# Performance work log

Hardware: AMD Instinct MI355X
Metric: run time of the kernel (lower is better)

## Reference

```python
import jax, jax.numpy as jnp
import numpy as np

N_NODES = 50000
N_EDGES = 800000
N_FEAT = 128
HIDDEN = 256
BN_EPS = 1e-5


def setup_inputs() -> dict:
    key = jax.random.key(0)
    ks = jax.random.split(key, 8)
    x = jax.random.normal(ks[0], (N_NODES, N_FEAT), dtype=jnp.float32)
    edge_index = jax.random.randint(ks[1], (2, N_EDGES), 0, N_NODES, dtype=jnp.int64)
    # Xavier-uniform linear weights (as in weights_init), zero biases
    def xavier(k, fan_in, fan_out):
        lim = float(np.sqrt(6.0 / (fan_in + fan_out)))
        return jax.random.uniform(k, (fan_in, fan_out), jnp.float32, -lim, lim)
    return {
        "x": x,
        "edge_index": edge_index,
        "W1": xavier(ks[2], N_FEAT, HIDDEN),
        "b1": jnp.zeros((HIDDEN,), jnp.float32),
        "g1": jnp.ones((HIDDEN,), jnp.float32),
        "be1": jnp.zeros((HIDDEN,), jnp.float32),
        "W2": xavier(ks[3], HIDDEN, HIDDEN),
        "b2": jnp.zeros((HIDDEN,), jnp.float32),
        "g2": jnp.ones((HIDDEN,), jnp.float32),
        "be2": jnp.zeros((HIDDEN,), jnp.float32),
        "Wfc": xavier(ks[4], HIDDEN, HIDDEN),
        "bfc": jnp.zeros((HIDDEN,), jnp.float32),
    }


def gcn_conv(x, src, dst, deg_inv_sqrt, W, b):
    """PyG GCNConv: out_i = sum_{j->i} d_i^-1/2 d_j^-1/2 (x_j W) + b,
    with self-loops already appended to (src, dst)."""
    h = x @ W                                        # [N, out]
    norm = deg_inv_sqrt[src] * deg_inv_sqrt[dst]     # [E+N]
    msgs = h[src] * norm[:, None]                    # gather + scale
    out = jax.ops.segment_sum(msgs, dst, num_segments=x.shape[0])
    return out + b


def batch_norm(x, gamma, beta):
    # training-mode BatchNorm1d: batch stats over nodes, biased variance
    mean = jnp.mean(x, axis=0)
    var = jnp.mean(jnp.square(x - mean), axis=0)
    return (x - mean) * jax.lax.rsqrt(var + BN_EPS) * gamma + beta


def reference(x, edge_index, W1, b1, g1, be1, W2, b2, g2, be2, Wfc, bfc):
    n = x.shape[0]
    loop = jnp.arange(n, dtype=edge_index.dtype)
    src = jnp.concatenate([edge_index[0], loop])
    dst = jnp.concatenate([edge_index[1], loop])
    deg = jax.ops.segment_sum(jnp.ones_like(src, dtype=x.dtype), dst, num_segments=n)
    deg_inv_sqrt = jnp.where(deg > 0, jax.lax.rsqrt(jnp.maximum(deg, 1.0)), 0.0)

    h = gcn_conv(x, src, dst, deg_inv_sqrt, W1, b1)
    h = batch_norm(h, g1, be1)
    # dropout is identity in deterministic (eval) reference
    h = gcn_conv(h, src, dst, deg_inv_sqrt, W2, b2)
    h = batch_norm(h, g2, be2)
    return h @ Wfc + bfc
```

## Files before the change

### kernel.cpp

```cpp
#include <hip/hip_runtime.h>
#include <hip/hip_bf16.h>

#define NFEAT 128
#define HID 256
#define BN_EPS 1e-5f
#define NBIN 64

typedef __attribute__((ext_vector_type(8))) __bf16 bf16x8;
typedef __attribute__((ext_vector_type(4))) float f32x4;

static __device__ __forceinline__ float bflo(unsigned u) {
    union { unsigned x; float f; } c; c.x = u << 16; return c.f;
}
static __device__ __forceinline__ float bfhi(unsigned u) {
    union { unsigned x; float f; } c; c.x = u & 0xffff0000u; return c.f;
}

__global__ void k_count(const int* __restrict__ ei, int E, int* __restrict__ cnt,
                        int* __restrict__ rank) {
    int e = blockIdx.x * blockDim.x + threadIdx.x;
    if (e < E) rank[e] = atomicAdd(&cnt[ei[E + e]], 1);
}

__global__ void k_scan1(const int* __restrict__ cnt, int n, int* __restrict__ partial,
                        int* __restrict__ blk_total) {
    __shared__ int sh[256];
    int i = blockIdx.x * 256 + threadIdx.x;
    int v = (i < n) ? cnt[i] : 0;
    sh[threadIdx.x] = v;
    __syncthreads();
    for (int off = 1; off < 256; off <<= 1) {
        int x = (threadIdx.x >= off) ? sh[threadIdx.x - off] : 0;
        __syncthreads();
        sh[threadIdx.x] += x;
        __syncthreads();
    }
    if (i < n) partial[i] = sh[threadIdx.x] - v;
    if (threadIdx.x == 255) blk_total[blockIdx.x] = sh[255];
}

__global__ void k_finalize(const int* __restrict__ partial, const int* __restrict__ blk_total,
                           const int* __restrict__ cnt, int n, int nblk,
                           int* __restrict__ row_start, float* __restrict__ dinv) {
    __shared__ int sw[4];
    const int t = threadIdx.x;
    const int b = blockIdx.x;
    int v = (t < b && t < nblk) ? blk_total[t] : 0;
#pragma unroll
    for (int m = 1; m < 64; m <<= 1) v += __shfl_xor(v, m);
    if ((t & 63) == 0) sw[t >> 6] = v;
    __syncthreads();
    int pref = sw[0] + sw[1] + sw[2] + sw[3];
    int i = b * 256 + t;
    if (i < n) {
        row_start[i] = partial[i] + pref;
        dinv[i] = rsqrtf((float)(cnt[i] + 1));
    }
}

__global__ void k_fill(const int* __restrict__ ei, const int* __restrict__ rank,
                       const int* __restrict__ row_start, int E, int* __restrict__ col) {
    int e = blockIdx.x * blockDim.x + threadIdx.x;
    if (e < E) {
        int d = ei[E + e];
        col[row_start[d] + rank[e]] = ei[e];
    }
}

__global__ void k_prep(const float* __restrict__ x, const float* __restrict__ dinv,
                       __hip_bfloat16* __restrict__ xs, const float* __restrict__ W1,
                       __hip_bfloat16* __restrict__ Wt1, int castBlocks, int n4) {
    int bid = blockIdx.x;
    int t = threadIdx.x;
    if (bid < castBlocks) {
        int i = bid * 256 + t;
        if (i < n4) {
            float d = dinv[i >> 5];
            float4 v = *(const float4*)(x + (size_t)i * 4);
            __hip_bfloat16* o = xs + (size_t)i * 4;
            o[0] = __float2bfloat16(v.x * d);
            o[1] = __float2bfloat16(v.y * d);
            o[2] = __float2bfloat16(v.z * d);
            o[3] = __float2bfloat16(v.w * d);
        }
    } else {
        int idx = (bid - castBlocks) * 256 + t;
        int n = idx & 255;
        int k = idx >> 8;
        Wt1[n * 128 + k] = __float2bfloat16(W1[k * 256 + n]);
    }
}

__global__ __launch_bounds__(256) void k_bnfoldW(const float* __restrict__ gs,
                                                 const float* __restrict__ g,
                                                 const float* __restrict__ be,
                                                 const float* __restrict__ b, float invN,
                                                 const float* __restrict__ W1,
                                                 const float* __restrict__ W2,
                                                 __hip_bfloat16* __restrict__ WfT,
                                                 float* __restrict__ uvec) {
    __shared__ float shs[256], shb[256];
    const int c = threadIdx.x;
    float s = 0.f, q = 0.f;
    for (int r = 0; r < NBIN; r++) {
        s += gs[r * 512 + c];
        q += gs[r * 512 + 256 + c];
    }
    float mean = s * invN;
    float var = q * invN - mean * mean;
    float scl = rsqrtf(var + BN_EPS) * g[c];
    shs[c] = scl;
    shb[c] = (b[c] - mean) * scl + be[c];
    __syncthreads();
    if (blockIdx.x < 128) {
        int k = blockIdx.x;
        float acc = 0.f;
        for (int m = 0; m < 256; m++) acc += W1[k * 256 + m] * shs[m] * W2[m * 256 + c];
        WfT[(size_t)c * 128 + k] = __float2bfloat16(acc);
    } else {
        float acc = 0.f;
        for (int m = 0; m < 256; m++) acc += W2[m * 256 + c] * shb[m];
        uvec[c] = acc;
    }
}

__global__ __launch_bounds__(256) void k_fold2(const float* __restrict__ gs,
                                               const float* __restrict__ g,
                                               const float* __restrict__ be, float invN,
                                               const float* __restrict__ Wfc,
                                               const float* __restrict__ bfc,
                                               __hip_bfloat16* __restrict__ Wtf,
                                               float* __restrict__ bias2) {
    __shared__ float shs[256], sho[256];
    const int c = threadIdx.x;
    float s = 0.f, q = 0.f;
    for (int r = 0; r < NBIN; r++) {
        s += gs[r * 512 + c];
        q += gs[r * 512 + 256 + c];
    }
    float mean = s * invN;
    float var = q * invN - mean * mean;
    float scl = rsqrtf(var + BN_EPS) * g[c];
    shs[c] = scl;
    sho[c] = (0.f - mean) * scl + be[c];
    __syncthreads();
    if (blockIdx.x < 256) {
        int k = blockIdx.x;
        Wtf[(size_t)c * 256 + k] = __float2bfloat16(Wfc[k * 256 + c] * shs[k]);
    } else {
        float acc = bfc[c];
        for (int m = 0; m < 256; m++) acc += sho[m] * Wfc[m * 256 + c];
        bias2[c] = acc;
    }
}

template <bool SCALE>
__global__ __launch_bounds__(256) void k_spmm(const __hip_bfloat16* __restrict__ Hs,
                                              const int* __restrict__ rs,
                                              const int* __restrict__ rc,
                                              const int* __restrict__ col,
                                              const float* __restrict__ dinv,
                                              __hip_bfloat16* __restrict__ out,
                                              float* __restrict__ rv, int N) {
    const int wid = blockIdx.x * 4 + (threadIdx.x >> 6);
    if (wid >= N) return;
    const int lane = threadIdx.x & 63;
    const int ch = lane * 2;
    const int s = rs[wid];
    const int deg = rc[wid];
    const float di = dinv[wid];

    unsigned u0 = *(const unsigned*)(Hs + (size_t)wid * 128 + ch);
    float a0, a1, dsum = 0.f;
    if constexpr (SCALE) { a0 = di * bflo(u0); a1 = di * bfhi(u0); }
    else { a0 = bflo(u0); a1 = bfhi(u0); }

    int e = 0;
    for (; e + 8 <= deg; e += 8) {
        int idx[8];
#pragma unroll
        for (int j = 0; j < 8; j++) idx[j] = col[s + e + j];
        float dj[8];
#pragma unroll
        for (int j = 0; j < 8; j++) dj[j] = dinv[idx[j]];
        unsigned u[8];
#pragma unroll
        for (int j = 0; j < 8; j++) u[j] = *(const unsigned*)(Hs + (size_t)idx[j] * 128 + ch);
#pragma unroll
        for (int j = 0; j < 8; j++) {
            if constexpr (SCALE) { a0 += dj[j] * bflo(u[j]); a1 += dj[j] * bfhi(u[j]); }
            else { a0 += bflo(u[j]); a1 += bfhi(u[j]); dsum += dj[j]; }
        }
    }
    for (; e < deg; e++) {
        int i0 = col[s + e];
        float d0 = dinv[i0];
        unsigned uu = *(const unsigned*)(Hs + (size_t)i0 * 128 + ch);
        if constexpr (SCALE) { a0 += d0 * bflo(uu); a1 += d0 * bfhi(uu); }
        else { a0 += bflo(uu); a1 += bfhi(uu); dsum += d0; }
    }
    union { unsigned w; unsigned short us[2]; } o;
    __hip_bfloat16 b0 = __float2bfloat16(di * a0); o.us[0] = *(unsigned short*)&b0;
    __hip_bfloat16 b1 = __float2bfloat16(di * a1); o.us[1] = *(unsigned short*)&b1;
    *(unsigned*)(out + (size_t)wid * 128 + ch) = o.w;
    if (!SCALE && rv && lane == 0) rv[wid] = di * (di + dsum);
}

template <int K, bool STATS>
__global__ __launch_bounds__(256, 4) void k_gemm2(const __hip_bfloat16* __restrict__ A,
                                                  const __hip_bfloat16* __restrict__ Bt,
                                                  const float* __restrict__ bias,
                                                  __hip_bfloat16* __restrict__ outb,
                                                  float* __restrict__ outf,
                                                  float* __restrict__ gs,
                                                  const float* __restrict__ rvec,
                                                  const float* __restrict__ uvec, int M) {
    constexpr int NC = K / 64;
    constexpr int LDR = 72;
    __shared__ __align__(16) unsigned short Bs[2 * 128 * LDR];
    float* sred = (float*)Bs;
    float* qred = sred + 512;

    const int t = threadIdx.x;
    const int wv = t >> 6;
    const int lane = t & 63;
    const int mlane = lane & 15;
    const int quad = lane >> 4;
    const int m0 = blockIdx.x * 128;
    const int n0 = blockIdx.y * 128;
    const int arow0 = m0 + wv * 32 + mlane;

    auto stage = [&](int c, int buf) {
#pragma unroll
        for (int i = 0; i < 4; i++) {
            int idx = t + i * 256;
            int row = idx >> 3;
            int c4 = idx & 7;
            uint4 v = *(const uint4*)(Bt + (size_t)(n0 + row) * K + c * 64 + c4 * 8);
            *(uint4*)(Bs + buf * (128 * LDR) + row * LDR + c4 * 8) = v;
        }
    };
    auto loadA = [&](int c, bf16x8 (&dst)[2][2]) {
#pragma unroll
        for (int mt = 0; mt < 2; mt++)
#pragma unroll
            for (int ks = 0; ks < 2; ks++)
                dst[mt][ks] = *(const bf16x8*)(A + (size_t)(arow0 + mt * 16) * K + c * 64 +
                                               ks * 32 + quad * 8);
    };

    f32x4 acc[2][8];
#pragma unroll
    for (int mt = 0; mt < 2; mt++)
#pragma unroll
        for (int i = 0; i < 8; i++) acc[mt][i] = (f32x4){0.f, 0.f, 0.f, 0.f};

    bf16x8 aP[2][2], aQ[2][2];
    loadA(0, aP);
    stage(0, 0);

    auto mmachunk = [&](int c, bf16x8 (&ac)[2][2]) {
        const unsigned short* base = Bs + (c & 1) * (128 * LDR);
#pragma unroll
        for (int nt = 0; nt < 8; nt++) {
            const unsigned short* bp = base + (nt * 16 + mlane) * LDR + quad * 8;
#pragma unroll
            for (int ks = 0; ks < 2; ks++) {
                bf16x8 b = *(const bf16x8*)(bp + ks * 32);
                acc[0][nt] = __builtin_amdgcn_mfma_f32_16x16x32_bf16(ac[0][ks], b, acc[0][nt], 0, 0, 0);
                acc[1][nt] = __builtin_amdgcn_mfma_f32_16x16x32_bf16(ac[1][ks], b, acc[1][nt], 0, 0, 0);
            }
        }
    };

#pragma unroll
    for (int c = 0; c < NC; c++) {
        __syncthreads();
        if (c + 1 < NC) {
            stage(c + 1, (c + 1) & 1);
            if ((c & 1) == 0) loadA(c + 1, aQ); else loadA(c + 1, aP);
        }
        if ((c & 1) == 0) mmachunk(c, aP); else mmachunk(c, aQ);
    }

    float rv[2][4] = {{0.f, 0.f, 0.f, 0.f}, {0.f, 0.f, 0.f, 0.f}};
    if (rvec) {
#pragma unroll
        for (int mt = 0; mt < 2; mt++)
#pragma unroll
            for (int r = 0; r < 4; r++) {
                int row = m0 + wv * 32 + mt * 16 + quad * 4 + r;
                if (row < M) rv[mt][r] = rvec[row];
            }
    }
    float sp[8], qp[8];
#pragma unroll
    for (int nt = 0; nt < 8; nt++) {
        int colx = n0 + nt * 16 + mlane;
        float bv = bias[colx];
        float uvn = uvec ? uvec[colx] : 0.f;
        float s = 0.f, q = 0.f;
#pragma unroll
        for (int mt = 0; mt < 2; mt++)
#pragma unroll
            for (int r = 0; r < 4; r++) {
                int row = m0 + wv * 32 + mt * 16 + quad * 4 + r;
                if (row < M) {
                    float h = acc[mt][nt][r] + bv + rv[mt][r] * uvn;
                    if (outb) outb[(size_t)row * HID + colx] = __float2bfloat16(h);
                    if (outf) outf[(size_t)row * HID + colx] = h;
                    s += h;
                    q += h * h;
                }
            }
        sp[nt] = s;
        qp[nt] = q;
    }
    if constexpr (STATS) {
#pragma unroll
        for (int nt = 0; nt < 8; nt++) {
            sp[nt] += __shfl_xor(sp[nt], 16);
            sp[nt] += __shfl_xor(sp[nt], 32);
            qp[nt] += __shfl_xor(qp[nt], 16);
            qp[nt] += __shfl_xor(qp[nt], 32);
        }
        __syncthreads();
        if (quad == 0) {
#pragma unroll
            for (int nt = 0; nt < 8; nt++) {
                sred[wv * 128 + nt * 16 + mlane] = sp[nt];
                qred[wv * 128 + nt * 16 + mlane] = qp[nt];
            }
        }
        __syncthreads();
        if (t < 128) {
            float ss = sred[t] + sred[128 + t] + sred[256 + t] + sred[384 + t];
            float qq = qred[t] + qred[128 + t] + qred[256 + t] + qred[384 + t];
            float* bin = gs + (blockIdx.x & (NBIN - 1)) * 512;
            atomicAdd(&bin[n0 + t], ss);
            atomicAdd(&bin[256 + n0 + t], qq);
        }
    }
}

extern "C" void kernel_launch(void* const* d_in, const int* in_sizes, int n_in, void* d_out,
                              int out_size, void* d_ws, size_t ws_size, hipStream_t stream) {
    const float* x = (const float*)d_in[0];
    const int* ei = (const int*)d_in[1];
    const float* W1 = (const float*)d_in[2];
    const float* b1 = (const float*)d_in[3];
    const float* g1 = (const float*)d_in[4];
    const float* be1 = (const float*)d_in[5];
    const float* W2 = (const float*)d_in[6];
    const float* b2 = (const float*)d_in[7];
    const float* g2 = (const float*)d_in[8];
    const float* be2 = (const float*)d_in[9];
    const float* Wfc = (const float*)d_in[10];
    const float* bfc = (const float*)d_in[11];
    float* out = (float*)d_out;

    const int N = in_sizes[0] / NFEAT;
    const int E = in_sizes[1] / 2;
    const float invN = 1.0f / (float)N;

    char* ws = (char*)d_ws;
    size_t off = 0;
    auto alloc = [&](size_t bytes) -> void* {
        void* p = ws + off;
        off += (bytes + 255) & ~(size_t)255;
        return p;
    };
    int* row_cnt = (int*)alloc((size_t)N * 4);
    float* gs1 = (float*)alloc((size_t)NBIN * 512 * 4);
    float* gs2 = (float*)alloc((size_t)NBIN * 512 * 4);
    size_t zero_bytes = ((size_t)ws - (size_t)row_cnt) + off;
    int* partial = (int*)alloc((size_t)N * 4);
    int* row_start = (int*)alloc((size_t)N * 4);
    int* blk = (int*)alloc(256 * 4);
    float* dinv = (float*)alloc((size_t)N * 4);
    int* rank = (int*)alloc((size_t)E * 4);
    int* col_idx = (int*)alloc((size_t)E * 4);
    float* uvec = (float*)alloc(256 * 4);
    float* bias2 = (float*)alloc(256 * 4);
    float* rvec = (float*)alloc((size_t)(N + 128) * 4);
    __hip_bfloat16* Wt1 = (__hip_bfloat16*)alloc(256 * 128 * 2);
    __hip_bfloat16* Wtf = (__hip_bfloat16*)alloc(256 * 256 * 2);
    __hip_bfloat16* WfT = (__hip_bfloat16*)alloc(256 * 128 * 2);
    __hip_bfloat16* xs = (__hip_bfloat16*)alloc((size_t)(N + 128) * NFEAT * 2);
    __hip_bfloat16* aggX = (__hip_bfloat16*)alloc((size_t)(N + 128) * NFEAT * 2);
    __hip_bfloat16* h2 = (__hip_bfloat16*)alloc((size_t)(N + 128) * HID * 2);
    __hip_bfloat16* t2 = xs;

    hipMemsetAsync(row_cnt, 0, zero_bytes, stream);

    k_count<<<(E + 255) / 256, 256, 0, stream>>>(ei, E, row_cnt, rank);
    int nblk = (N + 255) / 256;
    k_scan1<<<nblk, 256, 0, stream>>>(row_cnt, N, partial, blk);
    k_finalize<<<nblk, 256, 0, stream>>>(partial, blk, row_cnt, N, nblk, row_start, dinv);
    k_fill<<<(E + 255) / 256, 256, 0, stream>>>(ei, rank, row_start, E, col_idx);

    int castBlocks = (N * NFEAT / 4 + 255) / 256;
    k_prep<<<castBlocks + 128, 256, 0, stream>>>(x, dinv, xs, W1, Wt1, castBlocks, N * NFEAT / 4);

    int sg = (N + 3) / 4;
    dim3 gg((N + 127) / 128, 2);
    k_spmm<false><<<sg, 256, 0, stream>>>(xs, row_start, row_cnt, col_idx, dinv, aggX, rvec, N);
    k_spmm<true><<<sg, 256, 0, stream>>>(aggX, row_start, row_cnt, col_idx, dinv, t2, nullptr, N);
    k_gemm2<NFEAT, true><<<gg, 256, 0, stream>>>(aggX, Wt1, b1, nullptr, nullptr, gs1,
                                                 nullptr, nullptr, N);
    k_bnfoldW<<<129, 256, 0, stream>>>(gs1, g1, be1, b1, invN, W1, W2, WfT, uvec);
    k_gemm2<NFEAT, true><<<gg, 256, 0, stream>>>(t2, WfT, b2, h2, nullptr, gs2,
                                                 rvec, uvec, N);
    k_fold2<<<257, 256, 0, stream>>>(gs2, g2, be2, invN, Wfc, bfc, Wtf, bias2);
    k_gemm2<HID, false><<<gg, 256, 0, stream>>>(h2, Wtf, bias2, nullptr, out, nullptr,
                                                nullptr, nullptr, N);
}
```

Measured before the change: 317.4 us.

## Merge independent fill/cast kernels and run layer-1 GEMM alongside second SpMM

Combines the CSR column fill with the bf16 cast/weight transpose into one launch. It also merges the layer-1 stats GEMM with the second SpMM into a single kernel, partitioned by block index, since both only read aggX. This cuts kernel launches and lets the compute-bound GEMM overlap the memory-bound gather. In exchange, the merged kernel carries the GEMM's LDS allocation and launch bounds for the SpMM blocks, which may affect occupancy.

```diff
diff --git a/kernel.cpp b/kernel.cpp
--- a/kernel.cpp
+++ b/kernel.cpp
@@ -58,22 +58,22 @@
     }
 }
 
-__global__ void k_fill(const int* __restrict__ ei, const int* __restrict__ rank,
-                       const int* __restrict__ row_start, int E, int* __restrict__ col) {
-    int e = blockIdx.x * blockDim.x + threadIdx.x;
-    if (e < E) {
-        int d = ei[E + e];
-        col[row_start[d] + rank[e]] = ei[e];
-    }
-}
-
-__global__ void k_prep(const float* __restrict__ x, const float* __restrict__ dinv,
-                       __hip_bfloat16* __restrict__ xs, const float* __restrict__ W1,
-                       __hip_bfloat16* __restrict__ Wt1, int castBlocks, int n4) {
-    int bid = blockIdx.x;
-    int t = threadIdx.x;
-    if (bid < castBlocks) {
-        int i = bid * 256 + t;
+__global__ void k_fillcast(int fillBlocks, int castBlocks, const int* __restrict__ ei,
+                           const int* __restrict__ rank, const int* __restrict__ row_start,
+                           int E, int* __restrict__ col, const float* __restrict__ x,
+                           const float* __restrict__ dinv, __hip_bfloat16* __restrict__ xs,
+                           int n4, const float* __restrict__ W1,
+                           __hip_bfloat16* __restrict__ Wt1) {
+    const int bid = blockIdx.x;
+    const int t = threadIdx.x;
+    if (bid < fillBlocks) {
+        int e = bid * 256 + t;
+        if (e < E) {
+            int d = ei[E + e];
+            col[row_start[d] + rank[e]] = ei[e];
+        }
+    } else if (bid < fillBlocks + castBlocks) {
+        int i = (bid - fillBlocks) * 256 + t;
         if (i < n4) {
             float d = dinv[i >> 5];
             float4 v = *(const float4*)(x + (size_t)i * 4);
@@ -84,10 +84,10 @@
             o[3] = __float2bfloat16(v.w * d);
         }
     } else {
-        int idx = (bid - castBlocks) * 256 + t;
-        int n = idx & 255;
+        int idx = (bid - fillBlocks - castBlocks) * 256 + t;
+        int nn = idx & 255;
         int k = idx >> 8;
-        Wt1[n * 128 + k] = __float2bfloat16(W1[k * 256 + n]);
+        Wt1[nn * 128 + k] = __float2bfloat16(W1[k * 256 + nn]);
     }
 }
 
@@ -155,6 +155,57 @@
 }
 
 template <bool SCALE>
+static __device__ __forceinline__ void spmm_body(int wid, const __hip_bfloat16* __restrict__ Hs,
+                                                 const int* __restrict__ rs,
+                                                 const int* __restrict__ rc,
+                                                 const int* __restrict__ col,
+                                                 const float* __restrict__ dinv,
+                                                 __hip_bfloat16* __restrict__ out,
+                                                 float* __restrict__ rv, int N) {
+    if (wid >= N) return;
+    const int lane = threadIdx.x & 63;
+    const int ch = lane * 2;
+    const int s = rs[wid];
+    const int deg = rc[wid];
+    const float di = dinv[wid];
+
+    unsigned u0 = *(const unsigned*)(Hs + (size_t)wid * 128 + ch);
+    float a0, a1, dsum = 0.f;
+    if constexpr (SCALE) { a0 = di * bflo(u0); a1 = di * bfhi(u0); }
+    else { a0 = bflo(u0); a1 = bfhi(u0); }
+
+    int e = 0;
+    for (; e + 8 <= deg; e += 8) {
+        int idx[8];
+#pragma unroll
+        for (int j = 0; j < 8; j++) idx[j] = col[s + e + j];
+        float dj[8];
+#pragma unroll
+        for (int j = 0; j < 8; j++) dj[j] = dinv[idx[j]];
+        unsigned u[8];
+#pragma unroll
+        for (int j = 0; j < 8; j++) u[j] = *(const unsigned*)(Hs + (size_t)idx[j] * 128 + ch);
+#pragma unroll
+        for (int j = 0; j < 8; j++) {
+            if constexpr (SCALE) { a0 += dj[j] * bflo(u[j]); a1 += dj[j] * bfhi(u[j]); }
+            else { a0 += bflo(u[j]); a1 += bfhi(u[j]); dsum += dj[j]; }
+        }
+    }
+    for (; e < deg; e++) {
+        int i0 = col[s + e];
+        float d0 = dinv[i0];
+        unsigned uu = *(const unsigned*)(Hs + (size_t)i0 * 128 + ch);
+        if constexpr (SCALE) { a0 += d0 * bflo(uu); a1 += d0 * bfhi(uu); }
+        else { a0 += bflo(uu); a1 += bfhi(uu); dsum += d0; }
+    }
+    union { unsigned w; unsigned short us[2]; } o;
+    __hip_bfloat16 b0 = __float2bfloat16(di * a0); o.us[0] = *(unsigned short*)&b0;
+    __hip_bfloat16 b1 = __float2bfloat16(di * a1); o.us[1] = *(unsigned short*)&b1;
+    *(unsigned*)(out + (size_t)wid * 128 + ch) = o.w;
+    if (!SCALE && rv && lane == 0) rv[wid] = di * (di + dsum);
+}
+
+template <bool SCALE>
 __global__ __launch_bounds__(256) void k_spmm(const __hip_bfloat16* __restrict__ Hs,
                                               const int* __restrict__ rs,
                                               const int* __restrict__ rc,
@@ -162,62 +213,21 @@
                                               const float* __restrict__ dinv,
                                               __hip_bfloat16* __restrict__ out,
                                               float* __restrict__ rv, int N) {
-    const int wid = blockIdx.x * 4 + (threadIdx.x >> 6);
-    if (wid >= N) return;
-    const int lane = threadIdx.x & 63;
-    const int ch = lane * 2;
-    const int s = rs[wid];
-    const int deg = rc[wid];
-    const float di = dinv[wid];
-
-    unsigned u0 = *(const unsigned*)(Hs + (size_t)wid * 128 + ch);
-    float a0, a1, dsum = 0.f;
-    if constexpr (SCALE) { a0 = di * bflo(u0); a1 = di * bfhi(u0); }
-    else { a0 = bflo(u0); a1 = bfhi(u0); }
-
-    int e = 0;
-    for (; e + 8 <= deg; e += 8) {
-        int idx[8];
-#pragma unroll
-        for (int j = 0; j < 8; j++) idx[j] = col[s + e + j];
-        float dj[8];
-#pragma unroll
-        for (int j = 0; j < 8; j++) dj[j] = dinv[idx[j]];
-        unsigned u[8];
-#pragma unroll
-        for (int j = 0; j < 8; j++) u[j] = *(const unsigned*)(Hs + (size_t)idx[j] * 128 + ch);
-#pragma unroll
-        for (int j = 0; j < 8; j++) {
-            if constexpr (SCALE) { a0 += dj[j] * bflo(u[j]); a1 += dj[j] * bfhi(u[j]); }
-            else { a0 += bflo(u[j]); a1 += bfhi(u[j]); dsum += dj[j]; }
-        }
-    }
-    for (; e < deg; e++) {
-        int i0 = col[s + e];
-        float d0 = dinv[i0];
-        unsigned uu = *(const unsigned*)(Hs + (size_t)i0 * 128 + ch);
-        if constexpr (SCALE) { a0 += d0 * bflo(uu); a1 += d0 * bfhi(uu); }
-        else { a0 += bflo(uu); a1 += bfhi(uu); dsum += d0; }
-    }
-    union { unsigned w; unsigned short us[2]; } o;
-    __hip_bfloat16 b0 = __float2bfloat16(di * a0); o.us[0] = *(unsigned short*)&b0;
-    __hip_bfloat16 b1 = __float2bfloat16(di * a1); o.us[1] = *(unsigned short*)&b1;
-    *(unsigned*)(out + (size_t)wid * 128 + ch) = o.w;
-    if (!SCALE && rv && lane == 0) rv[wid] = di * (di + dsum);
+    spmm_body<SCALE>(blockIdx.x * 4 + (threadIdx.x >> 6), Hs, rs, rc, col, dinv, out, rv, N);
 }
 
 template <int K, bool STATS>
-__global__ __launch_bounds__(256, 4) void k_gemm2(const __hip_bfloat16* __restrict__ A,
-                                                  const __hip_bfloat16* __restrict__ Bt,
-                                                  const float* __restrict__ bias,
-                                                  __hip_bfloat16* __restrict__ outb,
-                                                  float* __restrict__ outf,
-                                                  float* __restrict__ gs,
-                                                  const float* __restrict__ rvec,
-                                                  const float* __restrict__ uvec, int M) {
+static __device__ __forceinline__ void gemm_body(unsigned short* Bs, int bx, int by,
+                                                 const __hip_bfloat16* __restrict__ A,
+                                                 const __hip_bfloat16* __restrict__ Bt,
+                                                 const float* __restrict__ bias,
+                                                 __hip_bfloat16* __restrict__ outb,
+                                                 float* __restrict__ outf,
+                                                 float* __restrict__ gs,
+                                                 const float* __restrict__ rvec,
+                                                 const float* __restrict__ uvec, int M) {
     constexpr int NC = K / 64;
     constexpr int LDR = 72;
-    __shared__ __align__(16) unsigned short Bs[2 * 128 * LDR];
     float* sred = (float*)Bs;
     float* qred = sred + 512;
 
@@ -226,8 +236,8 @@
     const int lane = t & 63;
     const int mlane = lane & 15;
     const int quad = lane >> 4;
-    const int m0 = blockIdx.x * 128;
-    const int n0 = blockIdx.y * 128;
+    const int m0 = bx * 128;
+    const int n0 = by * 128;
     const int arow0 = m0 + wv * 32 + mlane;
 
     auto stage = [&](int c, int buf) {
@@ -336,10 +346,42 @@
         if (t < 128) {
             float ss = sred[t] + sred[128 + t] + sred[256 + t] + sred[384 + t];
             float qq = qred[t] + qred[128 + t] + qred[256 + t] + qred[384 + t];
-            float* bin = gs + (blockIdx.x & (NBIN - 1)) * 512;
+            float* bin = gs + (bx & (NBIN - 1)) * 512;
             atomicAdd(&bin[n0 + t], ss);
             atomicAdd(&bin[256 + n0 + t], qq);
         }
+    }
+}
+
+template <int K, bool STATS>
+__global__ __launch_bounds__(256, 4) void k_gemm2(const __hip_bfloat16* __restrict__ A,
+                                                  const __hip_bfloat16* __restrict__ Bt,
+                                                  const float* __restrict__ bias,
+                                                  __hip_bfloat16* __restrict__ outb,
+                                                  float* __restrict__ outf,
+                                                  float* __restrict__ gs,
+                                                  const float* __restrict__ rvec,
+                                                  const float* __restrict__ uvec, int M) {
+    __shared__ __align__(16) unsigned short Bs[2 * 128 * 72];
+    gemm_body<K, STATS>(Bs, blockIdx.x, blockIdx.y, A, Bt, bias, outb, outf, gs, rvec, uvec, M);
+}
+
+__global__ __launch_bounds__(256, 4) void k_mid(int gb, const __hip_bfloat16* __restrict__ aggX,
+                                                const __hip_bfloat16* __restrict__ Wt1,
+                                                const float* __restrict__ b1,
+                                                float* __restrict__ gs1,
+                                                const int* __restrict__ rs,
+                                                const int* __restrict__ rc,
+                                                const int* __restrict__ col,
+                                                const float* __restrict__ dinv,
+                                                __hip_bfloat16* __restrict__ t2, int N) {
+    __shared__ __align__(16) unsigned short Bs[2 * 128 * 72];
+    if ((int)blockIdx.x < gb) {
+        gemm_body<NFEAT, true>(Bs, blockIdx.x >> 1, blockIdx.x & 1, aggX, Wt1, b1,
+                               nullptr, nullptr, gs1, nullptr, nullptr, N);
+    } else {
+        spmm_body<true>((blockIdx.x - gb) * 4 + (threadIdx.x >> 6), aggX, rs, rc, col, dinv,
+                        t2, nullptr, N);
     }
 }
 
@@ -373,7 +415,7 @@
     int* row_cnt = (int*)alloc((size_t)N * 4);
     float* gs1 = (float*)alloc((size_t)NBIN * 512 * 4);
     float* gs2 = (float*)alloc((size_t)NBIN * 512 * 4);
-    size_t zero_bytes = ((size_t)ws - (size_t)row_cnt) + off;
+    size_t zero_bytes = off;
     int* partial = (int*)alloc((size_t)N * 4);
     int* row_start = (int*)alloc((size_t)N * 4);
     int* blk = (int*)alloc(256 * 4);
@@ -393,24 +435,26 @@
 
     hipMemsetAsync(row_cnt, 0, zero_bytes, stream);
 
-    k_count<<<(E + 255) / 256, 256, 0, stream>>>(ei, E, row_cnt, rank);
-    int nblk = (N + 255) / 256;
+    const int nblk = (N + 255) / 256;
+    const int fillBlocks = (E + 255) / 256;
+    const int castBlocks = (N * NFEAT / 4 + 255) / 256;
+
+    k_count<<<fillBlocks, 256, 0, stream>>>(ei, E, row_cnt, rank);
     k_scan1<<<nblk, 256, 0, stream>>>(row_cnt, N, partial, blk);
     k_finalize<<<nblk, 256, 0, stream>>>(partial, blk, row_cnt, N, nblk, row_start, dinv);
-    k_fill<<<(E + 255) / 256, 256, 0, stream>>>(ei, rank, row_start, E, col_idx);
-
-    int castBlocks = (N * NFEAT / 4 + 255) / 256;
-    k_prep<<<castBlocks + 128, 256, 0, stream>>>(x, dinv, xs, W1, Wt1, castBlocks, N * NFEAT / 4);
-
-    int sg = (N + 3) / 4;
+    k_fillcast<<<fillBlocks + castBlocks + 128, 256, 0, stream>>>(
+        fillBlocks, castBlocks, ei, rank, row_start, E, col_idx, x, dinv, xs,
+        N * NFEAT / 4, W1, Wt1);
+
+    const int sg = (N + 3) / 4;
     dim3 gg((N + 127) / 128, 2);
+    const int gb = ((N + 127) / 128) * 2;
+
     k_spmm<false><<<sg, 256, 0, stream>>>(xs, row_start, row_cnt, col_idx, dinv, aggX, rvec, N);
-    k_spmm<true><<<sg, 256, 0, stream>>>(aggX, row_start, row_cnt, col_idx, dinv, t2, nullptr, N);
-    k_gemm2<NFEAT, true><<<gg, 256, 0, stream>>>(aggX, Wt1, b1, nullptr, nullptr, gs1,
-                                                 nullptr, nullptr, N);
+    k_mid<<<gb + sg, 256, 0, stream>>>(gb, aggX, Wt1, b1, gs1, row_start, row_cnt, col_idx,
+                                       dinv, t2, N);
     k_bnfoldW<<<129, 256, 0, stream>>>(gs1, g1, be1, b1, invN, W1, W2, WfT, uvec);
-    k_gemm2<NFEAT, true><<<gg, 256, 0, stream>>>(t2, WfT, b2, h2, nullptr, gs2,
-                                                 rvec, uvec, N);
+    k_gemm2<NFEAT, true><<<gg, 256, 0, stream>>>(t2, WfT, b2, h2, nullptr, gs2, rvec, uvec, N);
     k_fold2<<<257, 256, 0, stream>>>(gs2, g2, be2, invN, Wfc, bfc, Wtf, bias2);
     k_gemm2<HID, false><<<gg, 256, 0, stream>>>(h2, Wtf, bias2, nullptr, out, nullptr,
                                                 nullptr, nullptr, N);
```

New measurement: 334.9 us. 5.5% more time.
